# Performance work log

Measured on AMD Instinct MI355X. Metric: run time of the kernel, lower is better.

Reference implementation:

```python
import jax, jax.numpy as jnp
import numpy as np

N, E, F = 50000, 400000, 32

_WN = ["w10","w11","w20","w21","w30","w31","w40","w41","wl01","wl02","wl1","wl2"]
_BN = ["b10","b11","b20","b21","b30","b31","b40","b41","bl01","bl02","bl1","bl2"]
_DIMS = [(4,F),(F,F),(2*F+F+4,F),(F,F),(6*F,F),(F,F),(6*F,F),(F,F),(F,F),(F,F),(F,4),(F,1)]


def _lin(key, fin, fout):
    kw, kb = jax.random.split(key)
    w = jax.random.normal(kw, (fin, fout), jnp.float32) / np.float32(np.sqrt(fin))
    b = jax.random.normal(kb, (fout,), jnp.float32) * 0.01
    return w, b


def setup_inputs() -> dict:
    key = jax.random.key(0)
    ks = jax.random.split(key, 5)
    inp = {}
    inp["x"] = jax.random.normal(ks[0], (N, 4), jnp.float32)
    inp["edge_index"] = jax.random.randint(ks[1], (2, E), 0, N, jnp.int32)
    inp["edge_attr"] = jax.random.normal(ks[2], (E, 4), jnp.float32)
    inp["beta"] = jax.random.normal(ks[3], (N, 3), jnp.float32)
    lkeys = jax.random.split(ks[4], len(_DIMS))
    for i, (fin, fout) in enumerate(_DIMS):
        w, b = _lin(lkeys[i], fin, fout)
        inp[_WN[i]] = w
        inp[_BN[i]] = b
    return inp


def reference(x, edge_index, edge_attr, beta,
              w10, b10, w11, b11, w20, b20, w21, b21,
              w30, b30, w31, b31, w40, b40, w41, b41,
              wl01, bl01, wl02, bl02, wl1, bl1, wl2, bl2):
    row, col = edge_index[0], edge_index[1]
    n = x.shape[0]

    def mlp2(m, w0, b0, w1, b1):
        return jax.nn.relu(m @ w0 + b0) @ w1 + b1

    def seg_mean(h):  # scatter-mean onto target nodes (row), dim_size=n
        s = jax.ops.segment_sum(h, row, num_segments=n)
        c = jax.ops.segment_sum(jnp.ones((h.shape[0], 1), h.dtype), row, num_segments=n)
        return s / jnp.maximum(c, 1.0)

    # conv1: x is zeros with dim 4 (<=5), so message = mlp0(edge_attr)
    e1 = mlp2(edge_attr, w10, b10, w11, b11)            # [E,32]
    x1 = jax.nn.relu(seg_mean(e1)); e1 = jax.nn.relu(e1)
    # conv2
    ea2 = jnp.concatenate([edge_attr, e1], axis=1)      # [E,36]
    e2 = mlp2(jnp.concatenate([x1[row], x1[col], ea2], axis=1), w20, b20, w21, b21)
    x2 = jax.nn.relu(seg_mean(e2)); e2 = jax.nn.relu(e2)
    # conv3
    x21 = jnp.concatenate([x2, x1], axis=1)             # [N,64]
    ea3 = jnp.concatenate([e2, e1], axis=1)             # [E,64]
    e3 = mlp2(jnp.concatenate([x21[row], x21[col], ea3], axis=1), w30, b30, w31, b31)
    x3 = jax.nn.relu(seg_mean(e3)); e3 = jax.nn.relu(e3)
    # conv4 (node aggregate x4 is never used downstream, so skipped)
    x32 = jnp.concatenate([x3, x2], axis=1)
    ea4 = jnp.concatenate([e3, e2], axis=1)
    e4 = jax.nn.relu(mlp2(jnp.concatenate([x32[row], x32[col], ea4], axis=1), w40, b40, w41, b41))
    # heads
    out01 = e4 @ wl01 + bl01
    out02 = e4 @ wl02 + bl02
    edge_x = out01 @ wl1 + bl1 + edge_attr
    edge_x = edge_x / jnp.maximum(jnp.linalg.norm(edge_x, axis=1, keepdims=True), 1e-12)
    probs = jax.nn.sigmoid(out02 @ wl2 + bl2)           # [E,1]
    return (probs, edge_x, beta)
```

## Files before the change

kernel.cpp:

```cpp
#include <hip/hip_runtime.h>
#include <hip/hip_bf16.h>

#define EE 400000
#define NN 50000
#define SCAN_NBLK ((NN + 1023) / 1024)
#define NTILES (EE / 16)
#define TPX (NTILES / 8)
#define NPTILES (NN / 16)
#define INIT_NBLK ((NN + 255) / 256)

typedef float f32x4 __attribute__((ext_vector_type(4)));
typedef __bf16 bf16x8 __attribute__((ext_vector_type(8)));
typedef unsigned int u32;
typedef unsigned int u32x4 __attribute__((ext_vector_type(4)));

static __device__ __forceinline__ bf16x8 u4_as_bf8(u32x4 u) {
  return __builtin_bit_cast(bf16x8, u);
}
static __device__ __forceinline__ u32 relu_pk2(u32 d) {
  u32 m = (d & 0x80008000u) >> 15;
  m ^= 0x00010001u;
  return d & ((m << 16) - m);
}
static __device__ __forceinline__ u32 pk2bf(float a, float b) {
  union { __bf16 h[2]; u32 w; } t;
  t.h[0] = (__bf16)a; t.h[1] = (__bf16)b;
  return t.w;
}

__global__ void init_pack_kernel(const float* __restrict__ w10, const float* __restrict__ w11,
                                 const float* __restrict__ w20, const float* __restrict__ w21,
                                 const float* __restrict__ w30, const float* __restrict__ w31,
                                 const float* __restrict__ w40, const float* __restrict__ w41,
                                 const float* __restrict__ wl01, const float* __restrict__ wl1,
                                 const float* __restrict__ wl02, const float* __restrict__ wl2,
                                 const float* __restrict__ bl01, const float* __restrict__ bl02,
                                 const float* __restrict__ bl1, const float* __restrict__ bl2,
                                 __bf16* __restrict__ pk,
                                 int* __restrict__ count, float* __restrict__ headw) {
  const int t = threadIdx.x;
  if (blockIdx.x >= 43) {
    int i = (blockIdx.x - 43) * 256 + t;
    if (i < NN) count[i] = 0;
    if (blockIdx.x == 43) {
      if (t < 4) {
        float s = bl1[t];
        for (int j = 0; j < 32; ++j) s += bl01[j] * wl1[j * 4 + t];
        headw[160 + t] = s;
      } else if (t == 4) {
        float s = bl2[0];
        for (int j = 0; j < 32; ++j) s += bl02[j] * wl2[j];
        headw[164] = s;
      }
    }
    return;
  }
  const int f = blockIdx.x;
  int stage, lf;
  const float *W0, *W1;
  if (f < 4)       { stage = 1; lf = f;      W0 = w10; W1 = w11; }
  else if (f < 14) { stage = 2; lf = f - 4;  W0 = w20; W1 = w21; }
  else if (f < 28) { stage = 3; lf = f - 14; W0 = w30; W1 = w31; }
  else             { stage = 4; lf = f - 28; W0 = w40; W1 = w41; }
#pragma unroll
  for (int u = 0; u < 2; ++u) {
    int idx = t * 2 + u;
    int lane = idx >> 3, i = idx & 7;
    int l15 = lane & 15, g = lane >> 4;
    int k = 8 * g + i;
    float v = 0.f;
    if (stage == 1) {
      if (lf < 2)      v = (k < 4) ? W0[k * 32 + lf * 16 + l15] : 0.f;
      else             v = W1[k * 32 + (lf - 2) * 16 + l15];
    } else if (stage == 2) {
      if (lf < 4)      { int part = lf >> 1, nb = lf & 1; v = W0[(part * 32 + k) * 32 + nb * 16 + l15]; }
      else if (lf < 6) { int nb = lf - 4; v = (k < 4) ? W0[(64 + k) * 32 + nb * 16 + l15] : 0.f; }
      else if (lf < 8) { int nb = lf - 6; v = W0[(68 + k) * 32 + nb * 16 + l15]; }
      else             { int nb = lf - 8; v = W1[k * 32 + nb * 16 + l15]; }
    } else {
      if (lf < 8)       { int part = lf >> 2, kb = (lf >> 1) & 1, nb = lf & 1;
                          v = W0[(part * 64 + kb * 32 + k) * 32 + nb * 16 + l15]; }
      else if (lf < 12) { int eb = (lf - 8) >> 1, nb = lf & 1;
                          v = W0[(128 + eb * 32 + k) * 32 + nb * 16 + l15]; }
      else if (lf < 14) { int nb = lf - 12; v = W1[k * 32 + nb * 16 + l15]; }
      else {
        if (l15 < 4)      { float s = 0.f; for (int j = 0; j < 32; ++j) s += wl01[k * 32 + j] * wl1[j * 4 + l15]; v = s; }
        else if (l15 == 4){ float s = 0.f; for (int j = 0; j < 32; ++j) s += wl02[k * 32 + j] * wl2[j]; v = s; }
      }
    }
    pk[f * 512 + idx] = (__bf16)v;
  }
}

__global__ void hist_kernel(const int* __restrict__ rowi, int* __restrict__ count) {
  int e = blockIdx.x * blockDim.x + threadIdx.x;
  if (e < EE) atomicAdd(&count[rowi[e]], 1);
}

__global__ void scanA_kernel(const int* __restrict__ count, int* __restrict__ offs,
                             int* __restrict__ partial) {
  __shared__ int lds[1024];
  const int t = threadIdx.x;
  const int i = blockIdx.x * 1024 + t;
  int v = (i < NN) ? count[i] : 0;
  lds[t] = v;
  __syncthreads();
  for (int off = 1; off < 1024; off <<= 1) {
    int u = (t >= off) ? lds[t - off] : 0;
    __syncthreads();
    lds[t] += u;
    __syncthreads();
  }
  int incl = lds[t];
  if (i < NN) offs[i] = incl - v;
  if (t == 1023) partial[blockIdx.x] = incl;
}

__global__ void scanB_kernel(const int* __restrict__ partial, int* __restrict__ offs,
                             int* __restrict__ cursor) {
  __shared__ int sbase;
  const int t = threadIdx.x;
  const int b = blockIdx.x;
  if (t < 64) {
    int s = 0;
    for (int j = t; j < b; j += 64) s += partial[j];
#pragma unroll
    for (int o = 32; o > 0; o >>= 1) s += __shfl_down(s, o);
    if (t == 0) sbase = s;
  }
  __syncthreads();
  const int base = sbase;
  const int i = b * 1024 + t;
  if (i < NN) {
    int o = offs[i] + base;
    offs[i] = o;
    cursor[i] = o;
  }
  if (b == 0 && t == 0) offs[NN] = EE;
}

__global__ void scatter_kernel(const int* __restrict__ rowi, const int* __restrict__ coli,
                               const float* __restrict__ eattr, int* __restrict__ cursor,
                               uint4* __restrict__ record, int* __restrict__ inv) {
  int e = blockIdx.x * blockDim.x + threadIdx.x;
  if (e >= EE) return;
  int r = rowi[e];
  int p = atomicAdd(&cursor[r], 1);
  inv[e] = p;
  const float4 v = *(const float4*)(eattr + (size_t)e * 4);
  uint4 rec;
  rec.x = (u32)r;
  rec.y = (u32)coli[e];
  rec.z = pk2bf(v.x, v.y);
  rec.w = pk2bf(v.z, v.w);
  record[p] = rec;
}

template <int NKB>
__launch_bounds__(256, 4)
__global__ void aggproj_kernel(const __bf16* __restrict__ esrc,
                               const int* __restrict__ offs,
                               const __bf16* __restrict__ pk,
                               const __bf16* __restrict__ xold,
                               __bf16* __restrict__ xfresh,
                               __bf16* __restrict__ ur, __bf16* __restrict__ uc) {
  __shared__ __align__(16) float hl[16 * 36];
  const int t = threadIdx.x;
  const int base = blockIdx.x * 16;

#pragma unroll
  for (int q = 0; q < 2; ++q) {
    int idx = q * 256 + t;
    int nl = idx >> 5, j = idx & 31;
    int n = base + nl;
    int a = offs[n], b = offs[n + 1];
    float s = 0.f;
    for (int e = a; e < b; ++e)
      s += (float)esrc[(size_t)e * 32 + j];
    float x = fmaxf(s / fmaxf((float)(b - a), 1.f), 0.f);
    hl[nl * 36 + j] = x;
    xfresh[(size_t)n * 32 + j] = (__bf16)x;
  }
  __syncthreads();

  const int lane = t & 63;
  const int wid = t >> 6;
  if (wid >= 2) return;
  const int l15 = lane & 15;
  const int g = lane >> 4;

  f32x4 o0 = {0, 0, 0, 0}, o1 = {0, 0, 0, 0};
#pragma unroll
  for (int kb = 0; kb < NKB; ++kb) {
    bf16x8 Bf0 = *(const bf16x8*)(pk + (size_t)((wid * NKB + kb) * 2 + 0) * 512 + lane * 8);
    bf16x8 Bf1 = *(const bf16x8*)(pk + (size_t)((wid * NKB + kb) * 2 + 1) * 512 + lane * 8);
    bf16x8 a;
    if (kb == 0) {
      f32x4 h0 = *(const f32x4*)&hl[l15 * 36 + 8 * g];
      f32x4 h1 = *(const f32x4*)&hl[l15 * 36 + 8 * g + 4];
#pragma unroll
      for (int i = 0; i < 4; ++i) { a[i] = (__bf16)h0[i]; a[i + 4] = (__bf16)h1[i]; }
    } else {
      a = *(const bf16x8*)(xold + (size_t)(base + l15) * 32 + 8 * g);
    }
    o0 = __builtin_amdgcn_mfma_f32_16x16x32_bf16(a, Bf0, o0, 0, 0, 0);
    o1 = __builtin_amdgcn_mfma_f32_16x16x32_bf16(a, Bf1, o1, 0, 0, 0);
  }
  __bf16* dst = (wid == 0) ? ur : uc;
#pragma unroll
  for (int r = 0; r < 4; ++r) {
    int m = 4 * g + r;
    size_t row = (size_t)(base + m) * 32;
    dst[row + l15]      = (__bf16)o0[r];
    dst[row + 16 + l15] = (__bf16)o1[r];
  }
}

template <int STAGE>
__launch_bounds__(256, 5)
__global__ void conv_kernel(const __bf16* __restrict__ pk,
                            const float* __restrict__ B0, const float* __restrict__ B1v,
                            const uint4* __restrict__ record,
                            const __bf16* __restrict__ ur,
                            const __bf16* __restrict__ uc,
                            const __bf16* __restrict__ ein1,
                            const __bf16* __restrict__ ein2,
                            __bf16* __restrict__ d1,
                            const float* __restrict__ headw,
                            float* __restrict__ tmpP, float* __restrict__ tmpEX) {
  constexpr int NEB  = (STAGE == 1) ? 1 : 2;
  constexpr int FEB  = (STAGE == 1) ? 0 : (STAGE == 2) ? 4 : 8;
  constexpr int FW1  = (STAGE == 1) ? 2 : (STAGE == 2) ? 8 : 12;
  __shared__ __align__(16) float ldsH[4 * 16 * 36];

  const int tid = threadIdx.x;
  const int lane = tid & 63;
  const int wid = tid >> 6;
  const int l15 = lane & 15;
  const int g = lane >> 4;

  bf16x8 Bf[NEB][2];
#pragma unroll
  for (int eb = 0; eb < NEB; ++eb)
#pragma unroll
    for (int nb = 0; nb < 2; ++nb)
      Bf[eb][nb] = *(const bf16x8*)(pk + (size_t)(FEB + eb * 2 + nb) * 512 + lane * 8);
  bf16x8 B2f[2];
#pragma unroll
  for (int nb = 0; nb < 2; ++nb)
    B2f[nb] = *(const bf16x8*)(pk + (size_t)(FW1 + nb) * 512 + lane * 8);

  bf16x8 I0, I1;
#pragma unroll
  for (int i = 0; i < 8; ++i) {
    int k = 8 * g + i;
    I0[i] = (k == l15)      ? (__bf16)1.0f : (__bf16)0.0f;
    I1[i] = (k == 16 + l15) ? (__bf16)1.0f : (__bf16)0.0f;
  }

  const float b0j0 = B0[l15], b0j1 = B0[l15 + 16];
  const float b1j0 = B1v[l15], b1j1 = B1v[l15 + 16];

  bf16x8 Bh;
  float bexc = 0.f, bp = 0.f;
  if (STAGE == 4) {
    Bh = *(const bf16x8*)(pk + (size_t)14 * 512 + lane * 8);
    if (l15 < 4) bexc = headw[160 + l15];
    bp = headw[164];
  }

  float* hl = &ldsH[wid * 576];

  const int xcd = blockIdx.x & 7;
  const int wloc = (blockIdx.x >> 3) * 4 + wid;
  const int nwl = (gridDim.x >> 3) * 4;
  for (int t0 = wloc; t0 < TPX; t0 += nwl) {
    const int t = xcd * TPX + t0;
    const int base = t * 16;
    const int p = base + l15;

    const uint4 rec = record[p];

    bf16x8 urf, ucf;
    if (STAGE >= 2) {
      int rid = (int)rec.x, cid = (int)rec.y;
      urf = *(const bf16x8*)(ur + (size_t)rid * 32 + 8 * g);
      ucf = *(const bf16x8*)(uc + (size_t)cid * 32 + 8 * g);
    }

    bf16x8 ae;
    if (STAGE <= 2) {
      u32x4 u = {0, 0, 0, 0};
      if (g == 0) { u.x = rec.z; u.y = rec.w; }
      ae = u4_as_bf8(u);
    }

    f32x4 a0a = {0,0,0,0}, a0b = {0,0,0,0}, a1a = {0,0,0,0}, a1b = {0,0,0,0};
    if (STAGE >= 2) {
      a0a = __builtin_amdgcn_mfma_f32_16x16x32_bf16(urf, I0, a0a, 0, 0, 0);
      a1a = __builtin_amdgcn_mfma_f32_16x16x32_bf16(urf, I1, a1a, 0, 0, 0);
      a0a = __builtin_amdgcn_mfma_f32_16x16x32_bf16(ucf, I0, a0a, 0, 0, 0);
      a1a = __builtin_amdgcn_mfma_f32_16x16x32_bf16(ucf, I1, a1a, 0, 0, 0);
    }
#pragma unroll
    for (int eb = 0; eb < NEB; ++eb) {
      bf16x8 a;
      if (STAGE == 1) {
        a = ae;
      } else if (STAGE == 2) {
        if (eb == 0) a = ae;
        else {
          u32x4 u = *(const u32x4*)(ein1 + (size_t)p * 32 + 8 * g);
          u.x = relu_pk2(u.x); u.y = relu_pk2(u.y); u.z = relu_pk2(u.z); u.w = relu_pk2(u.w);
          a = u4_as_bf8(u);
        }
      } else {
        const __bf16* src = (eb == 0) ? ein1 : ein2;
        u32x4 u = *(const u32x4*)(src + (size_t)p * 32 + 8 * g);
        u.x = relu_pk2(u.x); u.y = relu_pk2(u.y); u.z = relu_pk2(u.z); u.w = relu_pk2(u.w);
        a = u4_as_bf8(u);
      }
      a0b = __builtin_amdgcn_mfma_f32_16x16x32_bf16(a, Bf[eb][0], a0b, 0, 0, 0);
      a1b = __builtin_amdgcn_mfma_f32_16x16x32_bf16(a, Bf[eb][1], a1b, 0, 0, 0);
    }
    f32x4 acc0 = a0a + a0b, acc1 = a1a + a1b;

#pragma unroll
    for (int r = 0; r < 4; ++r) {
      int m = 4 * g + r;
      hl[m * 36 + l15]      = fmaxf(acc0[r] + b0j0, 0.f);
      hl[m * 36 + l15 + 16] = fmaxf(acc1[r] + b0j1, 0.f);
    }
    f32x4 h0 = *(const f32x4*)&hl[l15 * 36 + 8 * g];
    f32x4 h1 = *(const f32x4*)&hl[l15 * 36 + 8 * g + 4];
    bf16x8 a2;
#pragma unroll
    for (int i = 0; i < 4; ++i) { a2[i] = (__bf16)h0[i]; a2[i + 4] = (__bf16)h1[i]; }
    f32x4 o0 = {0,0,0,0}, o1 = {0,0,0,0};
    o0 = __builtin_amdgcn_mfma_f32_16x16x32_bf16(a2, B2f[0], o0, 0, 0, 0);
    o1 = __builtin_amdgcn_mfma_f32_16x16x32_bf16(a2, B2f[1], o1, 0, 0, 0);

    if (STAGE <= 3) {
#pragma unroll
      for (int r = 0; r < 4; ++r) {
        int m = 4 * g + r;
        size_t eo = (size_t)(base + m) * 32;
        d1[eo + l15]      = (__bf16)(o0[r] + b1j0);
        d1[eo + l15 + 16] = (__bf16)(o1[r] + b1j1);
      }
    } else {
#pragma unroll
      for (int r = 0; r < 4; ++r) {
        int m = 4 * g + r;
        hl[m * 36 + l15]      = fmaxf(o0[r] + b1j0, 0.f);
        hl[m * 36 + l15 + 16] = fmaxf(o1[r] + b1j1, 0.f);
      }
      f32x4 q0 = *(const f32x4*)&hl[l15 * 36 + 8 * g];
      f32x4 q1 = *(const f32x4*)&hl[l15 * 36 + 8 * g + 4];
      bf16x8 a3;
#pragma unroll
      for (int i = 0; i < 4; ++i) { a3[i] = (__bf16)q0[i]; a3[i + 4] = (__bf16)q1[i]; }
      f32x4 ho = {0,0,0,0};
      ho = __builtin_amdgcn_mfma_f32_16x16x32_bf16(a3, Bh, ho, 0, 0, 0);
#pragma unroll
      for (int r = 0; r < 4; ++r) {
        int m = 4 * g + r;
        int po = base + m;
        float s = ho[r];
        u32 zz = __shfl(rec.z, m);
        u32 ww = __shfl(rec.w, m);
        float v = 0.f, sq = 0.f;
        if (l15 < 4) {
          u32 wzw = (l15 & 2) ? ww : zz;
          u32 bits = (l15 & 1) ? (wzw & 0xffff0000u) : (wzw << 16);
          v = s + bexc + __uint_as_float(bits);
          sq = v * v;
        }
        sq += __shfl_xor(sq, 1);
        sq += __shfl_xor(sq, 2);
        if (l15 < 4) tmpEX[(size_t)po * 4 + l15] = v * (1.f / fmaxf(sqrtf(sq), 1e-12f));
        if (l15 == 4) tmpP[po] = 1.f / (1.f + __expf(-(s + bp)));
      }
    }
  }
}

__global__ void unpermute_kernel(const int* __restrict__ inv,
                                 const float* __restrict__ tmpP,
                                 const float* __restrict__ tmpEX,
                                 const float* __restrict__ beta,
                                 float* __restrict__ outP, float* __restrict__ outEX,
                                 float* __restrict__ outB) {
  int e = blockIdx.x * blockDim.x + threadIdx.x;
  if (e >= EE) return;
  int p = inv[e];
  outP[e] = tmpP[p];
  float4 ex = *(const float4*)(tmpEX + (size_t)p * 4);
  *(float4*)(outEX + (size_t)e * 4) = ex;
  if (e < NN * 3) outB[e] = beta[e];
}

extern "C" void kernel_launch(void* const* d_in, const int* in_sizes, int n_in,
                              void* d_out, int out_size, void* d_ws, size_t ws_size,
                              hipStream_t stream) {
  const float* eattr = (const float*)d_in[2];
  const float* beta = (const float*)d_in[3];
  const float* w10 = (const float*)d_in[4];  const float* b10 = (const float*)d_in[5];
  const float* w11 = (const float*)d_in[6];  const float* b11 = (const float*)d_in[7];
  const float* w20 = (const float*)d_in[8];  const float* b20 = (const float*)d_in[9];
  const float* w21 = (const float*)d_in[10]; const float* b21 = (const float*)d_in[11];
  const float* w30 = (const float*)d_in[12]; const float* b30 = (const float*)d_in[13];
  const float* w31 = (const float*)d_in[14]; const float* b31 = (const float*)d_in[15];
  const float* w40 = (const float*)d_in[16]; const float* b40 = (const float*)d_in[17];
  const float* w41 = (const float*)d_in[18]; const float* b41 = (const float*)d_in[19];
  const float* wl01 = (const float*)d_in[20]; const float* bl01 = (const float*)d_in[21];
  const float* wl02 = (const float*)d_in[22]; const float* bl02 = (const float*)d_in[23];
  const float* wl1 = (const float*)d_in[24];  const float* bl1 = (const float*)d_in[25];
  const float* wl2 = (const float*)d_in[26];  const float* bl2 = (const float*)d_in[27];
  const int* rowi = (const int*)d_in[1];
  const int* coli = rowi + EE;

  char* w = (char*)d_ws;
  auto alloc = [&](size_t bytes) {
    char* p = w;
    w += (bytes + 255) & ~(size_t)255;
    return p;
  };
  __bf16* e1b = (__bf16*)alloc((size_t)EE * 32 * 2);
  __bf16* e2b = (__bf16*)alloc((size_t)EE * 32 * 2);
  __bf16* e3b = (__bf16*)alloc((size_t)EE * 32 * 2);
  __bf16* ur  = (__bf16*)alloc((size_t)NN * 32 * 2);
  __bf16* uc  = (__bf16*)alloc((size_t)NN * 32 * 2);
  __bf16* x1b = (__bf16*)alloc((size_t)NN * 32 * 2);
  __bf16* x2b = (__bf16*)alloc((size_t)NN * 32 * 2);
  __bf16* x3b = (__bf16*)alloc((size_t)NN * 32 * 2);
  int* count = (int*)alloc(NN * 4);
  int* offs = (int*)alloc((NN + 1) * 4);
  int* cursor = (int*)alloc(NN * 4);
  int* inv = (int*)alloc(EE * 4);
  uint4* record = (uint4*)alloc((size_t)EE * 16);
  float* tmpP = (float*)alloc((size_t)EE * 4);
  float* tmpEX = (float*)alloc((size_t)EE * 4 * 4);
  float* headw = (float*)alloc(256 * 4);
  int* partial = (int*)alloc(512 * 4);
  __bf16* packw = (__bf16*)alloc((size_t)43 * 512 * 2);

  float* outP = (float*)d_out;
  float* outEX = outP + EE;
  float* outB = outP + (size_t)5 * EE;

  __bf16* pk1 = packw;
  __bf16* pk2 = packw + 4 * 512;
  __bf16* pk3 = packw + 14 * 512;
  __bf16* pk4 = packw + 28 * 512;

  init_pack_kernel<<<43 + INIT_NBLK, 256, 0, stream>>>(
      w10, w11, w20, w21, w30, w31, w40, w41, wl01, wl1, wl02, wl2,
      bl01, bl02, bl1, bl2, packw, count, headw);
  hist_kernel<<<(EE + 255) / 256, 256, 0, stream>>>(rowi, count);
  scanA_kernel<<<SCAN_NBLK, 1024, 0, stream>>>(count, offs, partial);
  scanB_kernel<<<SCAN_NBLK, 1024, 0, stream>>>(partial, offs, cursor);
  scatter_kernel<<<(EE + 255) / 256, 256, 0, stream>>>(rowi, coli, eattr, cursor,
                                                       record, inv);

  conv_kernel<1><<<2048, 256, 0, stream>>>(pk1, b10, b11, record,
                                           (const __bf16*)nullptr, (const __bf16*)nullptr,
                                           (const __bf16*)nullptr, (const __bf16*)nullptr, e1b,
                                           (const float*)nullptr, (float*)nullptr, (float*)nullptr);
  aggproj_kernel<1><<<NPTILES, 256, 0, stream>>>(e1b, offs, pk2,
                                                 (const __bf16*)nullptr, x1b, ur, uc);
  conv_kernel<2><<<2048, 256, 0, stream>>>(pk2, b20, b21, record,
                                           ur, uc, e1b, (const __bf16*)nullptr, e2b,
                                           (const float*)nullptr, (float*)nullptr, (float*)nullptr);
  aggproj_kernel<2><<<NPTILES, 256, 0, stream>>>(e2b, offs, pk3, x1b, x2b, ur, uc);
  conv_kernel<3><<<2048, 256, 0, stream>>>(pk3, b30, b31, record,
                                           ur, uc, e2b, e1b, e3b,
                                           (const float*)nullptr, (float*)nullptr, (float*)nullptr);
  aggproj_kernel<2><<<NPTILES, 256, 0, stream>>>(e3b, offs, pk4, x2b, x3b, ur, uc);
  conv_kernel<4><<<2048, 256, 0, stream>>>(pk4, b40, b41, record,
                                           ur, uc, e3b, e2b, (__bf16*)nullptr,
                                           headw, tmpP, tmpEX);
  unpermute_kernel<<<(EE + 255) / 256, 256, 0, stream>>>(inv, tmpP, tmpEX, beta,
                                                         outP, outEX, outB);
}
```

Measured before the change: 193.4 us.

## Fuse first-layer edge MLP into scatter kernel, drop conv stage 1

Each scatter thread now computes the stage-1 edge MLP (4->32 relu, 32->32) in fp32 scalar code, with weights staged in shared memory, and writes the bf16 result directly at its sorted position. The separate conv_kernel<1> launch, with its re-read of the records, is removed. This saves a kernel launch and a pass over the edge data, but puts about 1K FMAs per thread and 64 float registers into a scatter kernel that was previously atomic/memory bound. Occupancy and the 64-byte per-thread row writes could hurt.

After: 195.3 us (median of 2 runs). Within noise of the previous version (+1.0%).

```diff
diff --git a/kernel.cpp b/kernel.cpp
--- a/kernel.cpp
+++ b/kernel.cpp
@@ -141,19 +141,59 @@
 
 __global__ void scatter_kernel(const int* __restrict__ rowi, const int* __restrict__ coli,
                                const float* __restrict__ eattr, int* __restrict__ cursor,
-                               uint4* __restrict__ record, int* __restrict__ inv) {
-  int e = blockIdx.x * blockDim.x + threadIdx.x;
+                               const float* __restrict__ w10, const float* __restrict__ b10,
+                               const float* __restrict__ w11, const float* __restrict__ b11,
+                               uint4* __restrict__ record, int* __restrict__ inv,
+                               __bf16* __restrict__ e1b) {
+  __shared__ __align__(16) float lw10[128];
+  __shared__ __align__(16) float lw11[1024];
+  __shared__ float lb10[32], lb11[32];
+  const int t = threadIdx.x;
+  if (t < 128) lw10[t] = w10[t];
+  if (t < 32) { lb10[t] = b10[t]; lb11[t] = b11[t]; }
+  for (int i = t; i < 1024; i += 256) lw11[i] = w11[i];
+  __syncthreads();
+
+  int e = blockIdx.x * blockDim.x + t;
   if (e >= EE) return;
   int r = rowi[e];
   int p = atomicAdd(&cursor[r], 1);
   inv[e] = p;
-  const float4 v = *(const float4*)(eattr + (size_t)e * 4);
+  const float4 ea = *(const float4*)(eattr + (size_t)e * 4);
   uint4 rec;
   rec.x = (u32)r;
   rec.y = (u32)coli[e];
-  rec.z = pk2bf(v.x, v.y);
-  rec.w = pk2bf(v.z, v.w);
+  rec.z = pk2bf(ea.x, ea.y);
+  rec.w = pk2bf(ea.z, ea.w);
   record[p] = rec;
+
+  float h[32];
+#pragma unroll
+  for (int j = 0; j < 32; ++j)
+    h[j] = fmaxf(lb10[j] + ea.x * lw10[j] + ea.y * lw10[32 + j] +
+                 ea.z * lw10[64 + j] + ea.w * lw10[96 + j], 0.f);
+  float s[32];
+#pragma unroll
+  for (int j = 0; j < 32; ++j) s[j] = lb11[j];
+#pragma unroll
+  for (int k = 0; k < 32; ++k) {
+    float hk = h[k];
+    const f32x4* wr = (const f32x4*)&lw11[k * 32];
+#pragma unroll
+    for (int q = 0; q < 8; ++q) {
+      f32x4 wv = wr[q];
+      s[q * 4 + 0] += hk * wv[0];
+      s[q * 4 + 1] += hk * wv[1];
+      s[q * 4 + 2] += hk * wv[2];
+      s[q * 4 + 3] += hk * wv[3];
+    }
+  }
+  union { __bf16 b[32]; uint4 u[4]; } out;
+#pragma unroll
+  for (int j = 0; j < 32; ++j) out.b[j] = (__bf16)s[j];
+  uint4* dst = (uint4*)(e1b + (size_t)p * 32);
+#pragma unroll
+  for (int q = 0; q < 4; ++q) dst[q] = out.u[q];
 }
 
 template <int NKB>
@@ -228,9 +268,9 @@
                             __bf16* __restrict__ d1,
                             const float* __restrict__ headw,
                             float* __restrict__ tmpP, float* __restrict__ tmpEX) {
-  constexpr int NEB  = (STAGE == 1) ? 1 : 2;
-  constexpr int FEB  = (STAGE == 1) ? 0 : (STAGE == 2) ? 4 : 8;
-  constexpr int FW1  = (STAGE == 1) ? 2 : (STAGE == 2) ? 8 : 12;
+  constexpr int NEB  = 2;
+  constexpr int FEB  = (STAGE == 2) ? 4 : 8;
+  constexpr int FW1  = (STAGE == 2) ? 8 : 12;
   __shared__ __align__(16) float ldsH[4 * 16 * 36];
 
   const int tid = threadIdx.x;
@@ -281,33 +321,26 @@
 
     const uint4 rec = record[p];
 
-    bf16x8 urf, ucf;
-    if (STAGE >= 2) {
-      int rid = (int)rec.x, cid = (int)rec.y;
-      urf = *(const bf16x8*)(ur + (size_t)rid * 32 + 8 * g);
-      ucf = *(const bf16x8*)(uc + (size_t)cid * 32 + 8 * g);
-    }
+    int rid = (int)rec.x, cid = (int)rec.y;
+    bf16x8 urf = *(const bf16x8*)(ur + (size_t)rid * 32 + 8 * g);
+    bf16x8 ucf = *(const bf16x8*)(uc + (size_t)cid * 32 + 8 * g);
 
     bf16x8 ae;
-    if (STAGE <= 2) {
+    if (STAGE == 2) {
       u32x4 u = {0, 0, 0, 0};
       if (g == 0) { u.x = rec.z; u.y = rec.w; }
       ae = u4_as_bf8(u);
     }
 
     f32x4 a0a = {0,0,0,0}, a0b = {0,0,0,0}, a1a = {0,0,0,0}, a1b = {0,0,0,0};
-    if (STAGE >= 2) {
-      a0a = __builtin_amdgcn_mfma_f32_16x16x32_bf16(urf, I0, a0a, 0, 0, 0);
-      a1a = __builtin_amdgcn_mfma_f32_16x16x32_bf16(urf, I1, a1a, 0, 0, 0);
-      a0a = __builtin_amdgcn_mfma_f32_16x16x32_bf16(ucf, I0, a0a, 0, 0, 0);
-      a1a = __builtin_amdgcn_mfma_f32_16x16x32_bf16(ucf, I1, a1a, 0, 0, 0);
-    }
+    a0a = __builtin_amdgcn_mfma_f32_16x16x32_bf16(urf, I0, a0a, 0, 0, 0);
+    a1a = __builtin_amdgcn_mfma_f32_16x16x32_bf16(urf, I1, a1a, 0, 0, 0);
+    a0a = __builtin_amdgcn_mfma_f32_16x16x32_bf16(ucf, I0, a0a, 0, 0, 0);
+    a1a = __builtin_amdgcn_mfma_f32_16x16x32_bf16(ucf, I1, a1a, 0, 0, 0);
 #pragma unroll
     for (int eb = 0; eb < NEB; ++eb) {
       bf16x8 a;
-      if (STAGE == 1) {
-        a = ae;
-      } else if (STAGE == 2) {
+      if (STAGE == 2) {
         if (eb == 0) a = ae;
         else {
           u32x4 u = *(const u32x4*)(ein1 + (size_t)p * 32 + 8 * g);
@@ -449,7 +482,6 @@
   float* outEX = outP + EE;
   float* outB = outP + (size_t)5 * EE;
 
-  __bf16* pk1 = packw;
   __bf16* pk2 = packw + 4 * 512;
   __bf16* pk3 = packw + 14 * 512;
   __bf16* pk4 = packw + 28 * 512;
@@ -461,12 +493,9 @@
   scanA_kernel<<<SCAN_NBLK, 1024, 0, stream>>>(count, offs, partial);
   scanB_kernel<<<SCAN_NBLK, 1024, 0, stream>>>(partial, offs, cursor);
   scatter_kernel<<<(EE + 255) / 256, 256, 0, stream>>>(rowi, coli, eattr, cursor,
-                                                       record, inv);
-
-  conv_kernel<1><<<2048, 256, 0, stream>>>(pk1, b10, b11, record,
-                                           (const __bf16*)nullptr, (const __bf16*)nullptr,
-                                           (const __bf16*)nullptr, (const __bf16*)nullptr, e1b,
-                                           (const float*)nullptr, (float*)nullptr, (float*)nullptr);
+                                                       w10, b10, w11, b11,
+                                                       record, inv, e1b);
+
   aggproj_kernel<1><<<NPTILES, 256, 0, stream>>>(e1b, offs, pk2,
                                                  (const __bf16*)nullptr, x1b, ur, uc);
   conv_kernel<2><<<2048, 256, 0, stream>>>(pk2, b20, b21, record,
```
